# Optimization experiments

Measured on AMD Instinct MI355X. Metric: run time of the kernel, lower is better.

Reference implementation:

```python
import jax, jax.numpy as jnp
import numpy as np

E, D_IN, D_OUT = 8, 1024, 1024
B, S = 4, 2048

def setup_inputs() -> dict:
    key = jax.random.key(0)
    k_x, k_g, k_gb, k_w = jax.random.split(key, 4)
    x = jax.random.normal(k_x, (B, S, D_IN), dtype=jnp.float32)
    gate_w = jax.random.normal(k_g, (D_IN, E), dtype=jnp.float32) * 0.02
    gate_b = jax.random.normal(k_gb, (E,), dtype=jnp.float32) * 0.02
    expert_w = jax.random.normal(k_w, (E, D_IN, D_OUT), dtype=jnp.float32) * 0.02
    return {"x": x, "gate_w": gate_w, "gate_b": gate_b, "expert_w": expert_w}

def reference(x, gate_w, gate_b, expert_w):
    # gate: softmax over experts
    gate_score = jax.nn.softmax(x @ gate_w + gate_b, axis=-1)        # [B,S,E]
    # all-expert dense GEMM: [B,S,E,out]
    expert_out = jnp.einsum('bsi,eio->bseo', x, expert_w)
    # gate-weighted combine: [B,S,out]
    out = jnp.einsum('bse,bseo->bso', gate_score, expert_out)
    return out
```

## Files before the change

### kernel.cpp

```cpp
#include <hip/hip_runtime.h>
#include <hip/hip_bf16.h>
#include <cstdint>

#define TOKENS 8192
#define DIN 1024
#define DOUT 1024
#define NE 8

typedef __bf16 bf16;
typedef __attribute__((ext_vector_type(8))) __bf16 bf16x8;
typedef __attribute__((ext_vector_type(4))) float floatx4;
typedef __attribute__((ext_vector_type(2))) float floatx2;

__device__ __forceinline__ void async16(const void* gptr, void* lptr) {
  __builtin_amdgcn_global_load_lds(
      (const __attribute__((address_space(1))) void*)gptr,
      (__attribute__((address_space(3))) void*)lptr,
      16, 0, 0);
}

__global__ __launch_bounds__(256) void prep_kernel(
    const float* __restrict__ x, const float* __restrict__ gw,
    const float* __restrict__ gb, float* __restrict__ g,
    bf16* __restrict__ xb, const float* __restrict__ w,
    bf16* __restrict__ wt) {
  __shared__ __align__(16) float smem[NE * DIN];

  if (blockIdx.x < 512) {
    const int tid = threadIdx.x;
#pragma unroll
    for (int k = 0; k < 8; ++k) {
      const int base = (k * 256 + tid) * 4;
      const floatx4 v = *(const floatx4*)(gw + base);
#pragma unroll
      for (int m = 0; m < 4; ++m) {
        const int j = base + m;
        smem[(j & 7) * DIN + (j >> 3)] = v[m];
      }
    }
    __syncthreads();

    const int lane = tid & 63;
    const int wave = tid >> 6;
#pragma unroll
    for (int tt = 0; tt < 4; ++tt) {
      const int t = blockIdx.x * 16 + wave * 4 + tt;
      const float* xr = x + (size_t)t * DIN;
      bf16* xbr = xb + (size_t)t * DIN;

      float acc[NE];
#pragma unroll
      for (int e = 0; e < NE; ++e) acc[e] = 0.f;

#pragma unroll
      for (int it = 0; it < 4; ++it) {
        const int i = it * 256 + lane * 4;
        const floatx4 xv = *(const floatx4*)(xr + i);
        union { bf16 b[4]; uint64_t u; } cv;
#pragma unroll
        for (int m = 0; m < 4; ++m) cv.b[m] = (bf16)xv[m];
        *(uint64_t*)(xbr + i) = cv.u;
#pragma unroll
        for (int e = 0; e < NE; ++e) {
          const floatx4 wv = *(const floatx4*)(smem + e * DIN + i);
          acc[e] += xv[0] * wv[0] + xv[1] * wv[1] + xv[2] * wv[2] + xv[3] * wv[3];
        }
      }
#pragma unroll
      for (int e = 0; e < NE; ++e)
#pragma unroll
        for (int off = 32; off > 0; off >>= 1)
          acc[e] += __shfl_xor(acc[e], off, 64);

      float lg[NE];
      float mx = -3.0e38f;
#pragma unroll
      for (int e = 0; e < NE; ++e) { lg[e] = acc[e] + gb[e]; mx = fmaxf(mx, lg[e]); }
      float s = 0.f;
#pragma unroll
      for (int e = 0; e < NE; ++e) { lg[e] = __expf(lg[e] - mx); s += lg[e]; }
      const float inv = 1.f / s;
      if (lane == 0) {
        floatx4 o0, o1;
#pragma unroll
        for (int e = 0; e < 4; ++e) { o0[e] = lg[e] * inv; o1[e] = lg[e + 4] * inv; }
        *(floatx4*)(g + (size_t)t * NE) = o0;
        *(floatx4*)(g + (size_t)t * NE + 4) = o1;
      }
    }
  } else {
    float (*tile)[65] = (float(*)[65])smem;
    const int b = blockIdx.x - 512;
    const int e = b >> 8;
    const int i0 = ((b >> 4) & 15) * 64;
    const int o0 = (b & 15) * 64;
    const int tid = threadIdx.x;
    const int c4 = (tid & 15) * 4;
    const int r = tid >> 4;

    const float* src = w + ((size_t)e * DIN + i0) * DOUT + o0;
#pragma unroll
    for (int rr = r; rr < 64; rr += 16) {
      const floatx4 v = *(const floatx4*)(src + (size_t)rr * DOUT + c4);
      tile[rr][c4] = v[0]; tile[rr][c4 + 1] = v[1];
      tile[rr][c4 + 2] = v[2]; tile[rr][c4 + 3] = v[3];
    }
    __syncthreads();
    bf16* dst = wt + ((size_t)e * DOUT + o0) * DIN + i0;
#pragma unroll
    for (int rr = r; rr < 64; rr += 16) {
      union { bf16 b[4]; uint64_t u; } cv;
#pragma unroll
      for (int j = 0; j < 4; ++j) cv.b[j] = (bf16)tile[c4 + j][rr];
      *(uint64_t*)(dst + (size_t)rr * DIN + c4) = cv.u;
    }
  }
}

__global__ __launch_bounds__(256, 2) void moe_gemm(
    const bf16* __restrict__ xb, const bf16* __restrict__ wt,
    const float* __restrict__ g, float* __restrict__ out) {
  __shared__ __align__(16) bf16 As[128 * 128];
  __shared__ __align__(16) bf16 Bs[128 * 128];

  const int tid = threadIdx.x;
  const int c = blockIdx.x & 7;
  const int jj = blockIdx.x >> 3;
  const int bm = (c >> 1) * 16 + (jj & 15);
  const int bn = (c & 1) * 4 + (jj >> 4);
  const int lane = tid & 63;
  const int wave = tid >> 6;
  const int wm = wave >> 1, wn = wave & 1;
  const int lr = lane & 15, lq = lane >> 4;

  const int srow = tid >> 4;
  const int scol = (((tid & 15) ^ (srow & 7)) << 3);

  const bf16* agp = xb + ((size_t)(bm * 128 + srow)) * DIN + scol;
  bf16* const alp = As + tid * 8;
  bf16* const blp = Bs + tid * 8;

  const int kx = lr & 7;

  const floatx4 fzero = {0.f, 0.f, 0.f, 0.f};
  floatx4 accF[4][4];
#pragma unroll
  for (int im = 0; im < 4; ++im)
#pragma unroll
    for (int in = 0; in < 4; ++in) accF[im][in] = fzero;

  const int tok0 = bm * 128 + wm * 64;

  for (int e = 0; e < NE; ++e) {
    const bf16* bgp = wt + ((size_t)e << 20) +
                      ((size_t)(bn * 128 + srow)) * DIN + scol;
    floatx4 accE[4][4];
#pragma unroll
    for (int im = 0; im < 4; ++im)
#pragma unroll
      for (int in = 0; in < 4; ++in) accE[im][in] = fzero;

    for (int k0 = 0; k0 < DIN; k0 += 128) {
      __syncthreads();
#pragma unroll
      for (int j = 0; j < 8; ++j) {
        async16(agp + k0 + (size_t)(16 * j) * DIN, alp + j * 2048);
        async16(bgp + k0 + (size_t)(16 * j) * DIN, blp + j * 2048);
      }
      __syncthreads();

#pragma unroll
      for (int h = 0; h < 4; ++h) {
        const int kg = ((h * 4 + lq) ^ kx) << 3;
        bf16x8 av[4], bv[4];
#pragma unroll
        for (int im = 0; im < 4; ++im)
          av[im] = *(const bf16x8*)(As + (wm * 64 + im * 16 + lr) * 128 + kg);
#pragma unroll
        for (int in = 0; in < 4; ++in)
          bv[in] = *(const bf16x8*)(Bs + (wn * 64 + in * 16 + lr) * 128 + kg);
#pragma unroll
        for (int im = 0; im < 4; ++im)
#pragma unroll
          for (int in = 0; in < 4; ++in)
            accE[im][in] = __builtin_amdgcn_mfma_f32_16x16x32_bf16(
                av[im], bv[in], accE[im][in], 0, 0, 0);
      }
    }

#pragma unroll
    for (int im = 0; im < 4; ++im) {
      float gv[4];
#pragma unroll
      for (int r = 0; r < 4; ++r)
        gv[r] = g[(size_t)(tok0 + im * 16 + lq * 4 + r) * NE + e];
#pragma unroll
      for (int in = 0; in < 4; ++in)
#pragma unroll
        for (int r = 0; r < 4; ++r)
          accF[im][in][r] += gv[r] * accE[im][in][r];
    }
  }

#pragma unroll
  for (int im = 0; im < 4; ++im)
#pragma unroll
    for (int in = 0; in < 4; ++in) {
      const int col = bn * 128 + wn * 64 + in * 16 + lr;
#pragma unroll
      for (int r = 0; r < 4; ++r)
        out[(size_t)(tok0 + im * 16 + lq * 4 + r) * DOUT + col] =
            accF[im][in][r];
    }
}

extern "C" void kernel_launch(void* const* d_in, const int* in_sizes, int n_in,
                              void* d_out, int out_size, void* d_ws,
                              size_t ws_size, hipStream_t stream) {
  const float* x  = (const float*)d_in[0];
  const float* gw = (const float*)d_in[1];
  const float* gb = (const float*)d_in[2];
  const float* w  = (const float*)d_in[3];
  float* out = (float*)d_out;

  char* ws = (char*)d_ws;
  float* g  = (float*)ws;
  bf16* xb  = (bf16*)(ws + 262144);
  bf16* wt  = (bf16*)(ws + 262144 + (size_t)TOKENS * DIN * 2);

  prep_kernel<<<2560, 256, 0, stream>>>(x, gw, gb, g, xb, w, wt);
  moe_gemm<<<512, 256, 0, stream>>>(xb, wt, g, out);
}
```

Baseline: 238.7 us.

## Double-buffer LDS tiles with BK=64 and flatten expert/K loop into one pipeline

```diff
diff --git a/kernel.cpp b/kernel.cpp
--- a/kernel.cpp
+++ b/kernel.cpp
@@ -120,8 +120,8 @@
 __global__ __launch_bounds__(256, 2) void moe_gemm(
     const bf16* __restrict__ xb, const bf16* __restrict__ wt,
     const float* __restrict__ g, float* __restrict__ out) {
-  __shared__ __align__(16) bf16 As[128 * 128];
-  __shared__ __align__(16) bf16 Bs[128 * 128];
+  __shared__ __align__(16) bf16 As[2][128 * 64];
+  __shared__ __align__(16) bf16 Bs[2][128 * 64];
 
   const int tid = threadIdx.x;
   const int c = blockIdx.x & 7;
@@ -133,73 +133,105 @@
   const int wm = wave >> 1, wn = wave & 1;
   const int lr = lane & 15, lq = lane >> 4;
 
-  const int srow = tid >> 4;
-  const int scol = (((tid & 15) ^ (srow & 7)) << 3);
-
-  const bf16* agp = xb + ((size_t)(bm * 128 + srow)) * DIN + scol;
-  bf16* const alp = As + tid * 8;
-  bf16* const blp = Bs + tid * 8;
-
+  const int srow = tid >> 3;
+  const int scol = (((tid & 7) ^ (srow & 7)) << 3);
   const int kx = lr & 7;
 
+  const bf16* const agp = xb + (size_t)(bm * 128 + srow) * DIN + scol;
+  const bf16* const bgp = wt + (size_t)(bn * 128 + srow) * DIN + scol;
+
   const floatx4 fzero = {0.f, 0.f, 0.f, 0.f};
-  floatx4 accF[4][4];
+  floatx4 accF[4][4], accE[4][4];
 #pragma unroll
   for (int im = 0; im < 4; ++im)
 #pragma unroll
-    for (int in = 0; in < 4; ++in) accF[im][in] = fzero;
+    for (int in = 0; in < 4; ++in) { accF[im][in] = fzero; accE[im][in] = fzero; }
 
   const int tok0 = bm * 128 + wm * 64;
 
-  for (int e = 0; e < NE; ++e) {
-    const bf16* bgp = wt + ((size_t)e << 20) +
-                      ((size_t)(bn * 128 + srow)) * DIN + scol;
-    floatx4 accE[4][4];
+  {
+    bf16* const alp = &As[0][tid * 8];
+    bf16* const blp = &Bs[0][tid * 8];
+#pragma unroll
+    for (int j = 0; j < 4; ++j)
+      async16(agp + (size_t)(32 * j) * DIN, alp + j * 2048);
+#pragma unroll
+    for (int j = 0; j < 4; ++j)
+      async16(bgp + (size_t)(32 * j) * DIN, blp + j * 2048);
+  }
+  __syncthreads();
+
+  for (int t = 0; t < 128; ++t) {
+    const int cur = t & 1;
+    const bf16* const Ab = &As[cur][0];
+    const bf16* const Bb = &Bs[cur][0];
+
+    bf16x8 av[2][4], bv[2][4];
+#pragma unroll
+    for (int kk = 0; kk < 2; ++kk) {
+      const int kg = ((kk * 4 + lq) ^ kx) << 3;
+#pragma unroll
+      for (int im = 0; im < 4; ++im)
+        av[kk][im] = *(const bf16x8*)(Ab + (wm * 64 + im * 16 + lr) * 64 + kg);
+#pragma unroll
+      for (int in = 0; in < 4; ++in)
+        bv[kk][in] = *(const bf16x8*)(Bb + (wn * 64 + in * 16 + lr) * 64 + kg);
+    }
+
+    const int t1 = t + 1;
+    bf16* const alp = &As[cur ^ 1][tid * 8];
+    bf16* const blp = &Bs[cur ^ 1][tid * 8];
+    const size_t koff = (size_t)((t1 & 15) << 6);
+    if (t1 < 128) {
+#pragma unroll
+      for (int j = 0; j < 4; ++j)
+        async16(agp + koff + (size_t)(32 * j) * DIN, alp + j * 2048);
+    }
+
+    __builtin_amdgcn_s_setprio(1);
 #pragma unroll
     for (int im = 0; im < 4; ++im)
 #pragma unroll
-      for (int in = 0; in < 4; ++in) accE[im][in] = fzero;
-
-    for (int k0 = 0; k0 < DIN; k0 += 128) {
-      __syncthreads();
-#pragma unroll
-      for (int j = 0; j < 8; ++j) {
-        async16(agp + k0 + (size_t)(16 * j) * DIN, alp + j * 2048);
-        async16(bgp + k0 + (size_t)(16 * j) * DIN, blp + j * 2048);
-      }
-      __syncthreads();
-
-#pragma unroll
-      for (int h = 0; h < 4; ++h) {
-        const int kg = ((h * 4 + lq) ^ kx) << 3;
-        bf16x8 av[4], bv[4];
-#pragma unroll
-        for (int im = 0; im < 4; ++im)
-          av[im] = *(const bf16x8*)(As + (wm * 64 + im * 16 + lr) * 128 + kg);
+      for (int in = 0; in < 4; ++in)
+        accE[im][in] = __builtin_amdgcn_mfma_f32_16x16x32_bf16(
+            av[0][im], bv[0][in], accE[im][in], 0, 0, 0);
+    __builtin_amdgcn_s_setprio(0);
+
+    if (t1 < 128) {
+      const bf16* const bsrc = bgp + ((size_t)(t1 >> 4) << 20) + koff;
+#pragma unroll
+      for (int j = 0; j < 4; ++j)
+        async16(bsrc + (size_t)(32 * j) * DIN, blp + j * 2048);
+    }
+
+    __builtin_amdgcn_s_setprio(1);
+#pragma unroll
+    for (int im = 0; im < 4; ++im)
+#pragma unroll
+      for (int in = 0; in < 4; ++in)
+        accE[im][in] = __builtin_amdgcn_mfma_f32_16x16x32_bf16(
+            av[1][im], bv[1][in], accE[im][in], 0, 0, 0);
+    __builtin_amdgcn_s_setprio(0);
+
+    if ((t & 15) == 15) {
+      const int e = t >> 4;
+#pragma unroll
+      for (int im = 0; im < 4; ++im) {
+        float gv[4];
+#pragma unroll
+        for (int r = 0; r < 4; ++r)
+          gv[r] = g[(size_t)(tok0 + im * 16 + lq * 4 + r) * NE + e];
 #pragma unroll
         for (int in = 0; in < 4; ++in)
-          bv[in] = *(const bf16x8*)(Bs + (wn * 64 + in * 16 + lr) * 128 + kg);
-#pragma unroll
-        for (int im = 0; im < 4; ++im)
-#pragma unroll
-          for (int in = 0; in < 4; ++in)
-            accE[im][in] = __builtin_amdgcn_mfma_f32_16x16x32_bf16(
-                av[im], bv[in], accE[im][in], 0, 0, 0);
-      }
-    }
-
-#pragma unroll
-    for (int im = 0; im < 4; ++im) {
-      float gv[4];
-#pragma unroll
-      for (int r = 0; r < 4; ++r)
-        gv[r] = g[(size_t)(tok0 + im * 16 + lq * 4 + r) * NE + e];
-#pragma unroll
-      for (int in = 0; in < 4; ++in)
-#pragma unroll
-        for (int r = 0; r < 4; ++r)
-          accF[im][in][r] += gv[r] * accE[im][in][r];
-    }
+#pragma unroll
+          for (int r = 0; r < 4; ++r) {
+            accF[im][in][r] += gv[r] * accE[im][in][r];
+            accE[im][in][r] = 0.f;
+          }
+      }
+    }
+
+    __syncthreads();
   }
 
 #pragma unroll
```

Result: faster. 232.6 us (-2.6%).
